# Optimization experiments

Measured on AMD Instinct MI355X. Metric: run time of the kernel, lower is better.

Reference implementation:

```python
import jax, jax.numpy as jnp
import numpy as np

CTX = 5  # context_len

def z_vector(x, ctx):
    # x: [B, L, E] -> [B, L, ctx*E]; slot j holds embedding of token (idx + j - ctx//2), zero-padded at edges
    half = ctx // 2
    B, L, E = x.shape
    xp = jnp.pad(x, ((0, 0), (half, half), (0, 0)))
    return jnp.concatenate([xp[:, i:i + L, :] for i in range(ctx)], axis=-1)

def setup_inputs() -> dict:
    key = jax.random.key(0)
    kq, ka, kw, kb = jax.random.split(key, 4)
    B, LQ, LA, E, F = 256, 64, 256, 300, 512
    question = jax.random.normal(kq, (B, LQ, E), dtype=jnp.float32)
    answer = jax.random.normal(ka, (B, LA, E), dtype=jnp.float32)
    W = jax.random.normal(kw, (CTX * E, F), dtype=jnp.float32) * 0.02
    b = jax.random.normal(kb, (F,), dtype=jnp.float32) * 0.02
    return {"question": question, "answer": answer, "W": W, "b": b}

def reference(question, answer, W, b):
    # Conv2d(1, F, (ctx*E, 1)) over the full-height Z vector == per-position linear map
    def branch(x):
        z = z_vector(x, CTX)                       # [B, L, ctx*E]
        out = jnp.einsum('blk,kf->bfl', z, W)      # [B, F, L]
        return out + b[None, :, None]
    return branch(question), branch(answer)
```

## Files before the change

### kernel.cpp

```cpp
#include <hip/hip_runtime.h>

#define NB   256
#define E0   300
#define EP   304
#define F_   512
#define KP   1536
#define NKT  48
#define LQ_  64
#define LA_  256

typedef __attribute__((ext_vector_type(4))) float f32x4;
typedef __attribute__((ext_vector_type(8))) short short8;

#define XQ_ELEMS (NB * (LQ_ + 4) * EP)
#define XA_ELEMS (NB * (LA_ + 4) * EP)
#define WF_ELEMS (F_ * KP)
#define OUTQ_ELEMS ((size_t)NB * F_ * LQ_)
#define XROWS (NB * (LQ_ + 4) + NB * (LA_ + 4))
#define XPBLK 24928
#define WPBLK 3072

__device__ __forceinline__ unsigned short f2bf(float x) {
    unsigned int u = __float_as_uint(x);
    u = u + 0x7fffu + ((u >> 16) & 1u);
    return (unsigned short)(u >> 16);
}

__global__ void prep_all(const float* __restrict__ q, const float* __restrict__ a,
                         const float* __restrict__ W,
                         unsigned short* __restrict__ xq, unsigned short* __restrict__ xa,
                         unsigned short* __restrict__ wfr)
{
    const int bid = blockIdx.x;
    if (bid < XPBLK) {
        int idx = bid * 256 + threadIdx.x;
        int row = idx / 76;
        int col = idx - row * 76;
        const float* src;
        unsigned short* dst;
        bool valid;
        if (row < NB * (LQ_ + 4)) {
            int b = row / (LQ_ + 4), lp = row - b * (LQ_ + 4);
            dst = xq + (size_t)row * EP;
            valid = (lp >= 2 && lp < 2 + LQ_);
            src = q + ((size_t)b * LQ_ + (lp - 2)) * E0;
        } else {
            int r2 = row - NB * (LQ_ + 4);
            int b = r2 / (LA_ + 4), lp = r2 - b * (LA_ + 4);
            dst = xa + (size_t)r2 * EP;
            valid = (lp >= 2 && lp < 2 + LA_);
            src = a + ((size_t)b * LA_ + (lp - 2)) * E0;
        }
        unsigned long long pk = 0ull;
        if (valid && col < 75) {
            const float4 v = reinterpret_cast<const float4*>(src)[col];
            pk = (unsigned long long)f2bf(v.x)
               | ((unsigned long long)f2bf(v.y) << 16)
               | ((unsigned long long)f2bf(v.z) << 32)
               | ((unsigned long long)f2bf(v.w) << 48);
        }
        *reinterpret_cast<unsigned long long*>(dst + (size_t)col * 4) = pk;
    } else {
        int idx = (bid - XPBLK) * 256 + threadIdx.x;
        int j    = idx & 7;
        int lane = (idx >> 3) & 63;
        int chunk = idx >> 9;
        int kc = chunk % NKT;
        int tile16 = chunk / NKT;
        int f  = tile16 * 16 + (lane & 15);
        int kp = kc * 32 + (lane >> 4) * 8 + j;
        int jj = kp / EP;
        int e  = kp - jj * EP;
        float v = (kp < 5 * EP && e < E0) ? W[(size_t)(jj * E0 + e) * F_ + f] : 0.f;
        wfr[idx] = f2bf(v);
    }
}

__global__ __launch_bounds__(256, 2) void qa_gemm(
    const unsigned short* __restrict__ xq,
    const unsigned short* __restrict__ xa,
    const unsigned short* __restrict__ wfr,
    const float* __restrict__ bias,
    float* __restrict__ out)
{
    __shared__ __align__(16) unsigned short lds[2 * 16384];

    const int bid = blockIdx.x;
    const int wg  = (bid & 7) * 160 + (bid >> 3);

    const int ftBase = (wg & 1) * 256;
    const int lt     = wg >> 1;

    const unsigned short* xp;
    float* ob;
    int Mb, lsh, Lp;
    if (lt < 128) { Mb = lt * 128;         xp = xq; lsh = 6; Lp = LQ_ + 4; ob = out; }
    else          { Mb = (lt - 128) * 128; xp = xa; lsh = 8; Lp = LA_ + 4; ob = out + OUTQ_ELEMS; }
    const int Lv = 1 << lsh;

    const int tid  = threadIdx.x;
    const int lane = tid & 63;
    const int wid  = tid >> 6;
    const int lq   = lane >> 4;
    const int lr   = lane & 15;
    const int s_c  = (lane & 3) ^ ((lane >> 3) & 3);
    const int sub  = lane >> 2;
    const int dzA  = wid * 1024;
    const int dzB  = dzA + 512;

    const int mr0 = Mb + wid * 32 + sub;
    const int mr1 = mr0 + 16;
    const unsigned short* gZ0 = xp + (size_t)((mr0 >> lsh) * Lp + (mr0 & (Lv - 1))) * EP + s_c * 8;
    const unsigned short* gZ1 = xp + (size_t)((mr1 >> lsh) * Lp + (mr1 & (Lv - 1))) * EP + s_c * 8;

    const unsigned short* wpA0 = wfr + (size_t)((ftBase >> 4) + wid * 4 + 0) * NKT * 512 + lane * 8;
    const unsigned short* wpA1 = wfr + (size_t)((ftBase >> 4) + wid * 4 + 1) * NKT * 512 + lane * 8;
    const unsigned short* wpA2 = wfr + (size_t)((ftBase >> 4) + wid * 4 + 2) * NKT * 512 + lane * 8;
    const unsigned short* wpA3 = wfr + (size_t)((ftBase >> 4) + wid * 4 + 3) * NKT * 512 + lane * 8;
    const unsigned short* wpB0 = wpA0 + 512;
    const unsigned short* wpB1 = wpA1 + 512;
    const unsigned short* wpB2 = wpA2 + 512;
    const unsigned short* wpB3 = wpA3 + 512;

    const int cs = (lq ^ ((lr >> 1) & 3)) * 16;
    int zoff[8];
#pragma unroll
    for (int n = 0; n < 8; ++n) zoff[n] = (n * 16 + lr) * 64 + cs;

#define GLLDS(p, d) __builtin_amdgcn_global_load_lds(                               \
        (const __attribute__((address_space(1))) void*)(p),                         \
        (__attribute__((address_space(3))) void*)(d), 16, 0, 0)
#define ST8(T) do { const int rb = ((T) & 1) * 16384; const size_t ko = (size_t)(T) * 128; \
    _Pragma("unroll") for (int kb = 0; kb < 4; ++kb) {                              \
        GLLDS(gZ0 + ko + kb * 32, lds + rb + kb * 4096 + dzA);                      \
        GLLDS(gZ1 + ko + kb * 32, lds + rb + kb * 4096 + dzB); } } while (0)
#define WLOAD(dst, p) do {                                                           \
    asm volatile("global_load_dwordx4 %0, %1, off" : "=v"(dst) : "v"(p) : "memory"); \
    (p) += 1024; } while (0)
#define W4A do { WLOAD(wA[0], wpA0); WLOAD(wA[1], wpA1);                             \
                 WLOAD(wA[2], wpA2); WLOAD(wA[3], wpA3); } while (0)
#define W4B do { WLOAD(wB[0], wpB0); WLOAD(wB[1], wpB1);                             \
                 WLOAD(wB[2], wpB2); WLOAD(wB[3], wpB3); } while (0)
#define ZRD8(DST, BLK) do { _Pragma("unroll") for (int n = 0; n < 8; ++n)            \
    DST[n] = *(const short8*)(bbase + (BLK) * 8192 + zoff[n]); } while (0)
#define SB __builtin_amdgcn_sched_barrier(0)
#define FENCE(VM, LG) do {                                                           \
    asm volatile("s_waitcnt vmcnt(" #VM ") lgkmcnt(" #LG ")" ::: "memory"); SB; } while (0)
#define MFMA32K(WU, ZU) do { __builtin_amdgcn_s_setprio(1);                          \
    _Pragma("unroll") for (int mf = 0; mf < 4; ++mf)                                 \
    _Pragma("unroll") for (int nt = 0; nt < 8; ++nt)                                 \
        acc[mf][nt] = __builtin_amdgcn_mfma_f32_16x16x32_bf16(                       \
            WU[mf], ZU[nt], acc[mf][nt], 0, 0, 0);                                   \
    __builtin_amdgcn_s_setprio(0); SB; } while (0)

    f32x4 acc[4][8] = {};
    short8 zA[8], zB[8], wA[4], wB[4];

    W4A; W4B;
    ST8(0);
    asm volatile("s_waitcnt vmcnt(0)\n\ts_barrier" ::: "memory");

    for (int S = 0; S < 11; ++S) {
        ST8(S + 1);
        const char* bbase = (const char*)lds + (S & 1) * 32768;
        ZRD8(zA, 0); ZRD8(zB, 1);
        FENCE(8, 0);
        MFMA32K(wA, zA); W4A;
        MFMA32K(wB, zB); W4B;
        ZRD8(zA, 2); ZRD8(zB, 3);
        FENCE(0, 0);
        MFMA32K(wA, zA); W4A;
        MFMA32K(wB, zB); W4B;
        asm volatile("s_barrier" ::: "memory");
    }
    {
        const char* bbase = (const char*)lds + 32768;
        ZRD8(zA, 0); ZRD8(zB, 1);
        FENCE(0, 0);
        MFMA32K(wA, zA); W4A;
        MFMA32K(wB, zB); W4B;
        ZRD8(zA, 2); ZRD8(zB, 3);
        FENCE(0, 0);
        MFMA32K(wA, zA);
        MFMA32K(wB, zB);
    }

#undef MFMA32K
#undef FENCE
#undef SB
#undef ZRD8
#undef W4A
#undef W4B
#undef WLOAD
#undef ST8
#undef GLLDS

#pragma unroll
    for (int nt = 0; nt < 8; ++nt) {
        const int m = Mb + nt * 16 + lr;
        const int b = m >> lsh;
        const int l = m & (Lv - 1);
        float* orow = ob + ((size_t)b * F_ << lsh) + l;
#pragma unroll
        for (int mf = 0; mf < 4; ++mf) {
            const int f0 = ftBase + wid * 64 + mf * 16 + lq * 4;
            const f32x4 v = acc[mf][nt];
#pragma unroll
            for (int r = 0; r < 4; ++r)
                orow[(size_t)(f0 + r) << lsh] = v[r] + __ldg(&bias[f0 + r]);
        }
    }
}

extern "C" void kernel_launch(void* const* d_in, const int* in_sizes, int n_in,
                              void* d_out, int out_size, void* d_ws, size_t ws_size,
                              hipStream_t stream)
{
    const float* q    = (const float*)d_in[0];
    const float* a    = (const float*)d_in[1];
    const float* W    = (const float*)d_in[2];
    const float* bias = (const float*)d_in[3];
    float* out = (float*)d_out;

    unsigned short* xq  = (unsigned short*)d_ws;
    unsigned short* xa  = xq + XQ_ELEMS;
    unsigned short* wfr = xa + XA_ELEMS;

    prep_all<<<XPBLK + WPBLK, 256, 0, stream>>>(q, a, W, xq, xa, wfr);
    qa_gemm<<<1280, 256, 0, stream>>>(xq, xa, wfr, bias, out);
}
```

Baseline: 151.8 us.

## Fuse activation bf16 conversion and zero-padding into GEMM staging loads

Removes the separate pass that converted question/answer activations to padded bf16 buffers in workspace. The GEMM now loads fp32 rows straight from the inputs into registers, clamps the row index for context shifts with a validity mask for edge padding, converts to bf16 and writes to LDS itself. The goal is to drop a full read/write round trip of the activations and a large prep launch. In exchange it reads fp32 (twice the bytes) redundantly for each of the five context slots and both F halves, and adds conversion ALU work and register pressure to the main loop.

```diff
diff --git a/kernel.cpp b/kernel.cpp
--- a/kernel.cpp
+++ b/kernel.cpp
@@ -12,13 +12,8 @@
 typedef __attribute__((ext_vector_type(4))) float f32x4;
 typedef __attribute__((ext_vector_type(8))) short short8;
 
-#define XQ_ELEMS (NB * (LQ_ + 4) * EP)
-#define XA_ELEMS (NB * (LA_ + 4) * EP)
 #define WF_ELEMS (F_ * KP)
 #define OUTQ_ELEMS ((size_t)NB * F_ * LQ_)
-#define XROWS (NB * (LQ_ + 4) + NB * (LA_ + 4))
-#define XPBLK 24928
-#define WPBLK 3072
 
 __device__ __forceinline__ unsigned short f2bf(float x) {
     unsigned int u = __float_as_uint(x);
@@ -26,59 +21,25 @@
     return (unsigned short)(u >> 16);
 }
 
-__global__ void prep_all(const float* __restrict__ q, const float* __restrict__ a,
-                         const float* __restrict__ W,
-                         unsigned short* __restrict__ xq, unsigned short* __restrict__ xa,
-                         unsigned short* __restrict__ wfr)
+__global__ void prep_w2(const float* __restrict__ W, unsigned short* __restrict__ wfr)
 {
-    const int bid = blockIdx.x;
-    if (bid < XPBLK) {
-        int idx = bid * 256 + threadIdx.x;
-        int row = idx / 76;
-        int col = idx - row * 76;
-        const float* src;
-        unsigned short* dst;
-        bool valid;
-        if (row < NB * (LQ_ + 4)) {
-            int b = row / (LQ_ + 4), lp = row - b * (LQ_ + 4);
-            dst = xq + (size_t)row * EP;
-            valid = (lp >= 2 && lp < 2 + LQ_);
-            src = q + ((size_t)b * LQ_ + (lp - 2)) * E0;
-        } else {
-            int r2 = row - NB * (LQ_ + 4);
-            int b = r2 / (LA_ + 4), lp = r2 - b * (LA_ + 4);
-            dst = xa + (size_t)r2 * EP;
-            valid = (lp >= 2 && lp < 2 + LA_);
-            src = a + ((size_t)b * LA_ + (lp - 2)) * E0;
-        }
-        unsigned long long pk = 0ull;
-        if (valid && col < 75) {
-            const float4 v = reinterpret_cast<const float4*>(src)[col];
-            pk = (unsigned long long)f2bf(v.x)
-               | ((unsigned long long)f2bf(v.y) << 16)
-               | ((unsigned long long)f2bf(v.z) << 32)
-               | ((unsigned long long)f2bf(v.w) << 48);
-        }
-        *reinterpret_cast<unsigned long long*>(dst + (size_t)col * 4) = pk;
-    } else {
-        int idx = (bid - XPBLK) * 256 + threadIdx.x;
-        int j    = idx & 7;
-        int lane = (idx >> 3) & 63;
-        int chunk = idx >> 9;
-        int kc = chunk % NKT;
-        int tile16 = chunk / NKT;
-        int f  = tile16 * 16 + (lane & 15);
-        int kp = kc * 32 + (lane >> 4) * 8 + j;
-        int jj = kp / EP;
-        int e  = kp - jj * EP;
-        float v = (kp < 5 * EP && e < E0) ? W[(size_t)(jj * E0 + e) * F_ + f] : 0.f;
-        wfr[idx] = f2bf(v);
-    }
+    int idx = blockIdx.x * 256 + threadIdx.x;
+    int j    = idx & 7;
+    int lane = (idx >> 3) & 63;
+    int chunk = idx >> 9;
+    int kc = chunk % NKT;
+    int tile16 = chunk / NKT;
+    int f  = tile16 * 16 + (lane & 15);
+    int kp = kc * 32 + (lane >> 4) * 8 + j;
+    int jj = kp / EP;
+    int e  = kp - jj * EP;
+    float v = (kp < 5 * EP && e < E0) ? W[(size_t)(jj * E0 + e) * F_ + f] : 0.f;
+    wfr[idx] = f2bf(v);
 }
 
 __global__ __launch_bounds__(256, 2) void qa_gemm(
-    const unsigned short* __restrict__ xq,
-    const unsigned short* __restrict__ xa,
+    const float* __restrict__ xqf,
+    const float* __restrict__ xaf,
     const unsigned short* __restrict__ wfr,
     const float* __restrict__ bias,
     float* __restrict__ out)
@@ -91,11 +52,11 @@
     const int ftBase = (wg & 1) * 256;
     const int lt     = wg >> 1;
 
-    const unsigned short* xp;
+    const float* X;
     float* ob;
-    int Mb, lsh, Lp;
-    if (lt < 128) { Mb = lt * 128;         xp = xq; lsh = 6; Lp = LQ_ + 4; ob = out; }
-    else          { Mb = (lt - 128) * 128; xp = xa; lsh = 8; Lp = LA_ + 4; ob = out + OUTQ_ELEMS; }
+    int Mb, lsh;
+    if (lt < 128) { Mb = lt * 128;         X = xqf; lsh = 6; ob = out; }
+    else          { Mb = (lt - 128) * 128; X = xaf; lsh = 8; ob = out + OUTQ_ELEMS; }
     const int Lv = 1 << lsh;
 
     const int tid  = threadIdx.x;
@@ -103,15 +64,12 @@
     const int wid  = tid >> 6;
     const int lq   = lane >> 4;
     const int lr   = lane & 15;
-    const int s_c  = (lane & 3) ^ ((lane >> 3) & 3);
+    const int q4   = lane & 3;
     const int sub  = lane >> 2;
-    const int dzA  = wid * 1024;
-    const int dzB  = dzA + 512;
-
-    const int mr0 = Mb + wid * 32 + sub;
-    const int mr1 = mr0 + 16;
-    const unsigned short* gZ0 = xp + (size_t)((mr0 >> lsh) * Lp + (mr0 & (Lv - 1))) * EP + s_c * 8;
-    const unsigned short* gZ1 = xp + (size_t)((mr1 >> lsh) * Lp + (mr1 & (Lv - 1))) * EP + s_c * 8;
+    const int c8   = (q4 ^ ((sub >> 1) & 3)) * 8;
+
+    const int r0 = Mb + wid * 32 + sub, r1 = r0 + 16;
+    const int l0 = r0 & (Lv - 1),       l1 = r1 & (Lv - 1);
 
     const unsigned short* wpA0 = wfr + (size_t)((ftBase >> 4) + wid * 4 + 0) * NKT * 512 + lane * 8;
     const unsigned short* wpA1 = wfr + (size_t)((ftBase >> 4) + wid * 4 + 1) * NKT * 512 + lane * 8;
@@ -127,13 +85,6 @@
 #pragma unroll
     for (int n = 0; n < 8; ++n) zoff[n] = (n * 16 + lr) * 64 + cs;
 
-#define GLLDS(p, d) __builtin_amdgcn_global_load_lds(                               \
-        (const __attribute__((address_space(1))) void*)(p),                         \
-        (__attribute__((address_space(3))) void*)(d), 16, 0, 0)
-#define ST8(T) do { const int rb = ((T) & 1) * 16384; const size_t ko = (size_t)(T) * 128; \
-    _Pragma("unroll") for (int kb = 0; kb < 4; ++kb) {                              \
-        GLLDS(gZ0 + ko + kb * 32, lds + rb + kb * 4096 + dzA);                      \
-        GLLDS(gZ1 + ko + kb * 32, lds + rb + kb * 4096 + dzB); } } while (0)
 #define WLOAD(dst, p) do {                                                           \
     asm volatile("global_load_dwordx4 %0, %1, off" : "=v"(dst) : "v"(p) : "memory"); \
     (p) += 1024; } while (0)
@@ -141,11 +92,42 @@
                  WLOAD(wA[2], wpA2); WLOAD(wA[3], wpA3); } while (0)
 #define W4B do { WLOAD(wB[0], wpB0); WLOAD(wB[1], wpB1);                             \
                  WLOAD(wB[2], wpB2); WLOAD(wB[3], wpB3); } while (0)
+
+#define ZISSUE(RL, LL, T, FR, VL) do {                                               \
+    _Pragma("unroll") for (int kb = 0; kb < 4; ++kb) {                               \
+        const int kp = (T) * 128 + kb * 32 + c8;                                     \
+        const int j  = kp / 304;                                                     \
+        const int e  = kp - j * 304;                                                 \
+        const int dj = j - 2;                                                        \
+        const int lo = -(LL), hi = (Lv - 1) - (LL);                                  \
+        const int djc = dj < lo ? lo : (dj > hi ? hi : dj);                          \
+        VL[kb] = (dj == djc);                                                        \
+        const float* a1 = X + (size_t)((RL) + djc) * 300 + e;                        \
+        const float* a2 = (e == 296) ? a1 : a1 + 4;                                  \
+        asm volatile("global_load_dwordx4 %0, %1, off" : "=v"(FR[kb][0]) : "v"(a1) : "memory"); \
+        asm volatile("global_load_dwordx4 %0, %1, off" : "=v"(FR[kb][1]) : "v"(a2) : "memory"); \
+    } } while (0)
+
+#define CVTW(FR, VL, H, T) do {                                                      \
+    const int rbB = (((T) & 1) * 32768) + wid * 2048 + (H) * 1024 + lane * 16;       \
+    _Pragma("unroll") for (int kb = 0; kb < 4; ++kb) {                               \
+        unsigned int u0 = (unsigned)f2bf(FR[kb][0].x) | ((unsigned)f2bf(FR[kb][0].y) << 16); \
+        unsigned int u1 = (unsigned)f2bf(FR[kb][0].z) | ((unsigned)f2bf(FR[kb][0].w) << 16); \
+        unsigned int u2 = (unsigned)f2bf(FR[kb][1].x) | ((unsigned)f2bf(FR[kb][1].y) << 16); \
+        unsigned int u3 = (unsigned)f2bf(FR[kb][1].z) | ((unsigned)f2bf(FR[kb][1].w) << 16); \
+        uint4 uu;                                                                    \
+        uu.x = VL[kb] ? u0 : 0u; uu.y = VL[kb] ? u1 : 0u;                            \
+        uu.z = VL[kb] ? u2 : 0u; uu.w = VL[kb] ? u3 : 0u;                            \
+        *(uint4*)((char*)lds + rbB + kb * 8192) = uu;                                \
+    } } while (0)
+
 #define ZRD8(DST, BLK) do { _Pragma("unroll") for (int n = 0; n < 8; ++n)            \
     DST[n] = *(const short8*)(bbase + (BLK) * 8192 + zoff[n]); } while (0)
 #define SB __builtin_amdgcn_sched_barrier(0)
 #define FENCE(VM, LG) do {                                                           \
     asm volatile("s_waitcnt vmcnt(" #VM ") lgkmcnt(" #LG ")" ::: "memory"); SB; } while (0)
+#define FENCEV(VM) do {                                                              \
+    asm volatile("s_waitcnt vmcnt(" #VM ")" ::: "memory"); SB; } while (0)
 #define MFMA32K(WU, ZU) do { __builtin_amdgcn_s_setprio(1);                          \
     _Pragma("unroll") for (int mf = 0; mf < 4; ++mf)                                 \
     _Pragma("unroll") for (int nt = 0; nt < 8; ++nt)                                 \
@@ -155,23 +137,34 @@
 
     f32x4 acc[4][8] = {};
     short8 zA[8], zB[8], wA[4], wB[4];
+    float4 zf1[4][2], zf2[4][2];
+    int vl1[4], vl2[4];
 
     W4A; W4B;
-    ST8(0);
-    asm volatile("s_waitcnt vmcnt(0)\n\ts_barrier" ::: "memory");
+    ZISSUE(r0, l0, 0, zf1, vl1);
+    ZISSUE(r1, l1, 0, zf2, vl2);
+    FENCE(0, 0);
+    CVTW(zf1, vl1, 0, 0);
+    CVTW(zf2, vl2, 1, 0);
+    asm volatile("s_waitcnt lgkmcnt(0)\n\ts_barrier" ::: "memory");
 
     for (int S = 0; S < 11; ++S) {
-        ST8(S + 1);
         const char* bbase = (const char*)lds + (S & 1) * 32768;
+        ZISSUE(r0, l0, S + 1, zf1, vl1);
         ZRD8(zA, 0); ZRD8(zB, 1);
         FENCE(8, 0);
         MFMA32K(wA, zA); W4A;
         MFMA32K(wB, zB); W4B;
+        FENCEV(8);
+        CVTW(zf1, vl1, 0, S + 1);
+        ZISSUE(r1, l1, S + 1, zf2, vl2);
         ZRD8(zA, 2); ZRD8(zB, 3);
-        FENCE(0, 0);
+        FENCE(8, 0);
         MFMA32K(wA, zA); W4A;
         MFMA32K(wB, zB); W4B;
-        asm volatile("s_barrier" ::: "memory");
+        FENCEV(8);
+        CVTW(zf2, vl2, 1, S + 1);
+        asm volatile("s_waitcnt lgkmcnt(0)\n\ts_barrier" ::: "memory");
     }
     {
         const char* bbase = (const char*)lds + 32768;
@@ -186,14 +179,15 @@
     }
 
 #undef MFMA32K
+#undef FENCEV
 #undef FENCE
 #undef SB
 #undef ZRD8
+#undef CVTW
+#undef ZISSUE
 #undef W4A
 #undef W4B
 #undef WLOAD
-#undef ST8
-#undef GLLDS
 
 #pragma unroll
     for (int nt = 0; nt < 8; ++nt) {
@@ -222,10 +216,8 @@
     const float* bias = (const float*)d_in[3];
     float* out = (float*)d_out;
 
-    unsigned short* xq  = (unsigned short*)d_ws;
-    unsigned short* xa  = xq + XQ_ELEMS;
-    unsigned short* wfr = xa + XA_ELEMS;
-
-    prep_all<<<XPBLK + WPBLK, 256, 0, stream>>>(q, a, W, xq, xa, wfr);
-    qa_gemm<<<1280, 256, 0, stream>>>(xq, xa, wfr, bias, out);
-}
+    unsigned short* wfr = (unsigned short*)d_ws;
+
+    prep_w2<<<WF_ELEMS / 256, 256, 0, stream>>>(W, wfr);
+    qa_gemm<<<1280, 256, 0, stream>>>(q, a, wfr, bias, out);
+}
```

After: 494.2 us. +225.6%, slower.
